# Optimization experiments

Measured on AMD Instinct MI355X. Metric: run time of the kernel, lower is better.

Reference implementation:

```python
import jax, jax.numpy as jnp
import numpy as np

NUM_HEADS = 12
NUM_LANDMARKS = 64
PINV_ITERS = 6


def moore_penrose_iter_pinv(x, iters=PINV_ITERS):
    # x: [..., m, m]
    abs_x = jnp.abs(x)
    col = abs_x.sum(axis=-1)
    row = abs_x.sum(axis=-2)
    z = jnp.swapaxes(x, -1, -2) / (jnp.max(col) * jnp.max(row))
    I = jnp.eye(x.shape[-1], dtype=x.dtype)
    for _ in range(iters):
        xz = x @ z
        z = 0.25 * z @ (13.0 * I - xz @ (15.0 * I - xz @ (7.0 * I - xz)))
    return z


def setup_inputs() -> dict:
    key = jax.random.key(0)
    k1, k2, k3, k4 = jax.random.split(key, 4)
    B, N, C = 2, 2048, 768
    x = jax.random.normal(k1, (B, N, C), dtype=jnp.float32)
    w_qkv = jax.random.normal(k2, (3 * C, C), dtype=jnp.float32) * 0.02
    w_proj = jax.random.normal(k3, (C, C), dtype=jnp.float32) * 0.02
    b_proj = jax.random.normal(k4, (C,), dtype=jnp.float32) * 0.02
    return {"x": x, "w_qkv": w_qkv, "w_proj": w_proj, "b_proj": b_proj}


def reference(x, w_qkv, w_proj, b_proj):
    B, N, C = x.shape
    H = NUM_HEADS
    m = NUM_LANDMARKS
    d = C // H
    scale = d ** -0.5
    original_N = N

    rem = N % m
    if rem > 0:  # pad at the FRONT of the sequence, as in the torch code
        x = jnp.pad(x, ((0, 0), (m - rem, 0), (0, 0)))
        N = x.shape[1]

    qkv = x @ w_qkv.T  # [B, N, 3C]
    q, k, v = jnp.split(qkv, 3, axis=-1)
    # [B, N, C] -> [B, H, N, d]
    to_heads = lambda t: t.reshape(B, N, H, d).transpose(0, 2, 1, 3)
    q, k, v = to_heads(q), to_heads(k), to_heads(v)
    q = q * scale

    l = N // m  # segment length per landmark (N is a multiple of m after padding)
    # '(n l) d -> n d' mean over l: landmarks [B, H, m, d]
    q_landmarks = q.reshape(B, H, m, l, d).mean(axis=3)
    k_landmarks = k.reshape(B, H, m, l, d).mean(axis=3)

    sim1 = jnp.einsum('bhnd,bhmd->bhnm', q, k_landmarks)          # [B,H,N,m]
    sim2 = jnp.einsum('bhid,bhjd->bhij', q_landmarks, k_landmarks)  # [B,H,m,m]
    sim3 = jnp.einsum('bhmd,bhnd->bhmn', q_landmarks, k)          # [B,H,m,N]

    attn1 = jax.nn.softmax(sim1, axis=-1)
    attn2 = jax.nn.softmax(sim2, axis=-1)
    attn3 = jax.nn.softmax(sim3, axis=-1)

    attn2_inv = moore_penrose_iter_pinv(attn2, PINV_ITERS)

    attn = (attn1 @ attn2_inv) @ attn3            # [B,H,N,N] full attention map
    out = attn1 @ (attn2_inv @ (attn3 @ v))       # [B,H,N,d]

    out = out.transpose(0, 2, 1, 3).reshape(B, N, C)
    out = out[:, -original_N:]
    out = out @ w_proj.T + b_proj
    return out, attn
```

## Files before the change

### kernel.cpp

```cpp
#include <hip/hip_runtime.h>
#include <math.h>

#define BQ 2
#define NQ 2048
#define CQ 768
#define HQ 12
#define DQ 64
#define MQ 64
#define LQ 32
#define C3 2304
#define BH 24
#define BN 4096

typedef short bf16x8 __attribute__((ext_vector_type(8)));
typedef float f32x4 __attribute__((ext_vector_type(4)));

__device__ inline void atomicMaxPosF(float* addr, float v) {
  atomicMax((int*)addr, __float_as_int(v));
}

__device__ inline void f2pair(float f, ushort& hi, ushort& lo) {
  union { float f; unsigned u; } a; a.f = f;
  hi = (ushort)(a.u >> 16);
  union { unsigned u; float f; } h; h.u = ((unsigned)hi) << 16;
  union { float f; unsigned u; } b; b.f = f - h.f;
  lo = (ushort)(b.u >> 16);
}

__device__ inline int swzb(int row, int kbyte) {
  return row * 128 + (kbyte ^ ((row & 7) << 4));
}

__device__ inline bf16x8 ldfrag(const ushort* plane, int row, int kbyte) {
  return *(const bf16x8*)((const char*)plane + swzb(row, kbyte));
}

__device__ inline void stage_nt(const float* __restrict__ src, int ld,
                                ushort* ph, ushort* pl, int t) {
#pragma unroll
  for (int rep = 0; rep < 4; ++rep) {
    int idx = t + rep * 256;
    int row = idx >> 4, f4 = idx & 15;
    float4 v = *(const float4*)(src + (size_t)row * ld + f4 * 4);
    ushort h0, h1, h2, h3, l0, l1, l2, l3;
    f2pair(v.x, h0, l0); f2pair(v.y, h1, l1);
    f2pair(v.z, h2, l2); f2pair(v.w, h3, l3);
    int byt = row * 128 + ((f4 * 8) ^ ((row & 7) << 4));
    *(ushort4*)((char*)ph + byt) = make_ushort4(h0, h1, h2, h3);
    *(ushort4*)((char*)pl + byt) = make_ushort4(l0, l1, l2, l3);
  }
}

__device__ inline void stage_nn(const float* __restrict__ src, int ld,
                                ushort* ph, ushort* pl, int t) {
#pragma unroll
  for (int rep = 0; rep < 4; ++rep) {
    int idx = t + rep * 256;
    int krow = idx >> 4, f4 = idx & 15;
    float4 v = *(const float4*)(src + (size_t)krow * ld + f4 * 4);
    float vv[4] = {v.x, v.y, v.z, v.w};
#pragma unroll
    for (int c = 0; c < 4; ++c) {
      int n = f4 * 4 + c;
      ushort hi, lo;
      f2pair(vv[c], hi, lo);
      int byt = n * 128 + ((krow * 2) ^ ((n & 7) << 4));
      *(ushort*)((char*)ph + byt) = hi;
      *(ushort*)((char*)pl + byt) = lo;
    }
  }
}

__device__ inline void tile_mma(const ushort* Ah, const ushort* Al,
                                const ushort* Bh, const ushort* Bl,
                                f32x4 acc[2][2], int lane, int wm, int wn) {
  bf16x8 aH[2][2], aL[2][2], bH[2][2], bL[2][2];
#pragma unroll
  for (int mi = 0; mi < 2; ++mi)
#pragma unroll
    for (int ki = 0; ki < 2; ++ki) {
      int kb = ki * 64 + ((lane >> 4) * 16);
      int ra = wm * 32 + mi * 16 + (lane & 15);
      int rb = wn * 32 + mi * 16 + (lane & 15);
      aH[mi][ki] = ldfrag(Ah, ra, kb);
      aL[mi][ki] = ldfrag(Al, ra, kb);
      bH[mi][ki] = ldfrag(Bh, rb, kb);
      bL[mi][ki] = ldfrag(Bl, rb, kb);
    }
#pragma unroll
  for (int mi = 0; mi < 2; ++mi)
#pragma unroll
    for (int ni = 0; ni < 2; ++ni)
#pragma unroll
      for (int ki = 0; ki < 2; ++ki) {
        acc[mi][ni] = __builtin_amdgcn_mfma_f32_16x16x32_bf16(
            aH[mi][ki], bH[ni][ki], acc[mi][ni], 0, 0, 0);
        acc[mi][ni] = __builtin_amdgcn_mfma_f32_16x16x32_bf16(
            aH[mi][ki], bL[ni][ki], acc[mi][ni], 0, 0, 0);
        acc[mi][ni] = __builtin_amdgcn_mfma_f32_16x16x32_bf16(
            aL[mi][ki], bH[ni][ki], acc[mi][ni], 0, 0, 0);
      }
}

__global__ __launch_bounds__(256) void gemm_nt_mfma(
    const float* __restrict__ X, const float* __restrict__ W,
    const float* __restrict__ bias, float* __restrict__ Y,
    int Kdim, int ldx, int ldw, int ldy, int qscale)
{
  __shared__ __align__(16) ushort lds[16384];
  ushort* Ah = lds; ushort* Al = lds + 4096;
  ushort* Bh = lds + 8192; ushort* Bl = lds + 12288;
  const int t = threadIdx.x;
  const int r0 = blockIdx.x * 64, c0 = blockIdx.y * 64;
  const int lane = t & 63, wv = t >> 6, wm = wv >> 1, wn = wv & 1;
  f32x4 z = {0.f, 0.f, 0.f, 0.f};
  f32x4 acc[2][2] = {{z, z}, {z, z}};
  for (int k0 = 0; k0 < Kdim; k0 += 64) {
    stage_nt(X + (size_t)r0 * ldx + k0, ldx, Ah, Al, t);
    stage_nt(W + (size_t)c0 * ldw + k0, ldw, Bh, Bl, t);
    __syncthreads();
    tile_mma(Ah, Al, Bh, Bl, acc, lane, wm, wn);
    __syncthreads();
  }
#pragma unroll
  for (int mi = 0; mi < 2; ++mi)
#pragma unroll
    for (int ni = 0; ni < 2; ++ni) {
      int row = r0 + wm * 32 + mi * 16 + (lane >> 4) * 4;
      int col = c0 + wn * 32 + ni * 16 + (lane & 15);
      float badd = bias ? bias[col] : 0.0f;
      float sc = (qscale && col < CQ) ? 0.125f : 1.0f;
#pragma unroll
      for (int r = 0; r < 4; ++r)
        Y[(size_t)(row + r) * ldy + col] = acc[mi][ni][r] * sc + badd;
    }
}

__global__ __launch_bounds__(256) void gemm_heads_mfma(
    const float* __restrict__ A, const float* __restrict__ Bsrc,
    float* __restrict__ Cm,
    int kTilesPerSplit, int transB, int nBH,
    long long sAb, long long sAh, int lda,
    long long sBb, long long sBh, int ldb,
    long long sCb, long long sCh, int ldc, long long sCsplit)
{
  __shared__ __align__(16) ushort lds[16384];
  ushort* Ah = lds; ushort* Al = lds + 4096;
  ushort* Bh = lds + 8192; ushort* Bl = lds + 12288;
  const int t = threadIdx.x;
  const int z = blockIdx.z;
  const int split = z / nBH;
  const int bh = z % nBH;
  const int b = bh / HQ, h = bh % HQ;
  const float* Ap = A + (size_t)b * sAb + (size_t)h * sAh;
  const float* Bp = Bsrc + (size_t)b * sBb + (size_t)h * sBh;
  float* Cp = Cm + (size_t)b * sCb + (size_t)h * sCh + (size_t)split * sCsplit;
  const int m0 = blockIdx.x * 64, n0 = blockIdx.y * 64;
  const int lane = t & 63, wv = t >> 6, wm = wv >> 1, wn = wv & 1;
  f32x4 zz = {0.f, 0.f, 0.f, 0.f};
  f32x4 acc[2][2] = {{zz, zz}, {zz, zz}};
  const int kbase = split * kTilesPerSplit * 64;
  for (int kt = 0; kt < kTilesPerSplit; ++kt) {
    int k0 = kbase + kt * 64;
    stage_nt(Ap + (size_t)m0 * lda + k0, lda, Ah, Al, t);
    if (transB)
      stage_nt(Bp + (size_t)n0 * ldb + k0, ldb, Bh, Bl, t);
    else
      stage_nn(Bp + (size_t)k0 * ldb + n0, ldb, Bh, Bl, t);
    __syncthreads();
    tile_mma(Ah, Al, Bh, Bl, acc, lane, wm, wn);
    __syncthreads();
  }
#pragma unroll
  for (int mi = 0; mi < 2; ++mi)
#pragma unroll
    for (int ni = 0; ni < 2; ++ni) {
      int row = m0 + wm * 32 + mi * 16 + (lane >> 4) * 4;
      int col = n0 + wn * 32 + ni * 16 + (lane & 15);
#pragma unroll
      for (int r = 0; r < 4; ++r)
        Cp[(size_t)(row + r) * ldc + col] = acc[mi][ni][r];
    }
}

__global__ void landmarks_kernel(const float* __restrict__ qkv,
                                 float* __restrict__ ql, float* __restrict__ kl)
{
  int idx = blockIdx.x * 256 + threadIdx.x;
  int sel = idx / 98304;
  int r = idx % 98304;
  int bh = r / 4096;
  int b = bh / HQ, h = bh % HQ;
  int i = (r % 4096) / 64;
  int dd = r & 63;
  const float* base = qkv + (size_t)(b * NQ + i * LQ) * C3 + sel * CQ + h * 64 + dd;
  float s = 0.f;
#pragma unroll
  for (int j = 0; j < LQ; ++j) s += base[(size_t)j * C3];
  float* outp = sel ? kl : ql;
  outp[bh * 4096 + i * 64 + dd] = s * (1.0f / 32.0f);
}

__global__ __launch_bounds__(256) void attn2_prep(
    const float* __restrict__ ql, const float* __restrict__ kl,
    float* __restrict__ attn2, float* __restrict__ scal)
{
  __shared__ float Q[64][68], Kl[64][68], S[64][68];
  __shared__ float red[128];
  const int bh = blockIdx.x;
  const int t = threadIdx.x;
#pragma unroll
  for (int rep = 0; rep < 4; ++rep) {
    int idx = t + rep * 256;
    int row = idx >> 4, f4 = idx & 15;
    *(float4*)&Q[row][f4 * 4] = *(const float4*)(ql + (size_t)bh * 4096 + row * 64 + f4 * 4);
    *(float4*)&Kl[row][f4 * 4] = *(const float4*)(kl + (size_t)bh * 4096 + row * 64 + f4 * 4);
  }
  __syncthreads();
  {
    int i = t >> 2;
    int jb = (t & 3) * 16;
    for (int jj = 0; jj < 16; ++jj) {
      int j = jb + jj;
      float s2 = 0.f;
#pragma unroll
      for (int kk = 0; kk < 64; ++kk) s2 = fmaf(Q[i][kk], Kl[j][kk], s2);
      S[i][j] = s2;
    }
  }
  __syncthreads();
  if (t < 64) {
    float mx = -INFINITY;
    for (int j = 0; j < 64; ++j) mx = fmaxf(mx, S[t][j]);
    float sum = 0.f;
    for (int j = 0; j < 64; ++j) { float e = expf(S[t][j] - mx); S[t][j] = e; sum += e; }
    float inv = 1.0f / sum;
    float rs = 0.f;
    for (int j = 0; j < 64; ++j) { float v = S[t][j] * inv; S[t][j] = v; rs += v; }
    red[t] = rs;
  }
  __syncthreads();
  if (t < 64) {
    float cs = 0.f;
    for (int i = 0; i < 64; ++i) cs += S[i][t];
    red[64 + t] = cs;
  }
  __syncthreads();
  if (t == 0) {
    float m1 = red[0], m2 = red[64];
    for (int j = 1; j < 64; ++j) { m1 = fmaxf(m1, red[j]); m2 = fmaxf(m2, red[64 + j]); }
    atomicMaxPosF(scal + 0, m1);
    atomicMaxPosF(scal + 1, m2);
  }
  for (int idx = t; idx < 4096; idx += 256)
    attn2[(size_t)bh * 4096 + idx] = S[idx >> 6][idx & 63];
}

__device__ inline void mm64x(float (*D)[68], const float (*A)[68], const float (*B)[68],
                             int t, float scale)
{
  const int lane = t & 63, wv = t >> 6;
  float bcol[64];
#pragma unroll
  for (int kk = 0; kk < 64; ++kk) bcol[kk] = B[kk][lane];
#pragma unroll
  for (int rr = 0; rr < 4; ++rr) {
    int i = wv * 4 + rr;
    float acc2 = 0.f;
#pragma unroll
    for (int kk = 0; kk < 64; ++kk) acc2 = fmaf(A[i][kk], bcol[kk], acc2);
    D[i][lane] = acc2 * scale;
  }
}

__global__ __launch_bounds__(1024) void pinv_kernel(
    const float* __restrict__ attn2, const float* __restrict__ scal,
    float* __restrict__ zinv)
{
  __shared__ float X[64][68], Z[64][68], P[64][68], Q[64][68], R[64][68];
  const int bh = blockIdx.x;
  const int t = threadIdx.x;
  const float denom = scal[0] * scal[1];
#pragma unroll
  for (int rep = 0; rep < 4; ++rep) {
    int idx = t + rep * 1024;
    X[idx >> 6][idx & 63] = attn2[(size_t)bh * 4096 + idx];
  }
  __syncthreads();
#pragma unroll
  for (int rep = 0; rep < 4; ++rep) {
    int idx = t + rep * 1024;
    int i = idx >> 6, j = idx & 63;
    Z[j][i] = X[i][j] / denom;
  }
  for (int it = 0; it < 6; ++it) {
    __syncthreads();
    mm64x(P, X, Z, t, 1.0f);
    __syncthreads();
    for (int idx = t; idx < 4096; idx += 1024) {
      int i = idx >> 6, j = idx & 63;
      Q[i][j] = (i == j ? 7.0f : 0.0f) - P[i][j];
    }
    __syncthreads();
    mm64x(R, P, Q, t, 1.0f);
    __syncthreads();
    for (int idx = t; idx < 4096; idx += 1024) {
      int i = idx >> 6, j = idx & 63;
      Q[i][j] = (i == j ? 15.0f : 0.0f) - R[i][j];
    }
    __syncthreads();
    mm64x(R, P, Q, t, 1.0f);
    __syncthreads();
    for (int idx = t; idx < 4096; idx += 1024) {
      int i = idx >> 6, j = idx & 63;
      Q[i][j] = (i == j ? 13.0f : 0.0f) - R[i][j];
    }
    __syncthreads();
    mm64x(P, Z, Q, t, 0.25f);
    __syncthreads();
    for (int idx = t; idx < 4096; idx += 1024) {
      int i = idx >> 6, j = idx & 63;
      Z[i][j] = P[i][j];
    }
  }
  __syncthreads();
  for (int idx = t; idx < 4096; idx += 1024)
    zinv[(size_t)bh * 4096 + idx] = Z[idx >> 6][idx & 63];
}

__global__ __launch_bounds__(256) void attn1_kernel(
    const float* __restrict__ qkv, const float* __restrict__ kl,
    float* __restrict__ attn1)
{
  __shared__ float qs[64][68], klt[64][68];
  const int n0 = blockIdx.x * 64;
  const int bh = blockIdx.y;
  const int b = bh / HQ, h = bh % HQ;
  const int t = threadIdx.x;
#pragma unroll
  for (int rep = 0; rep < 4; ++rep) {
    int idx = t + rep * 256;
    int row = idx >> 4, f4 = idx & 15;
    *(float4*)&qs[row][f4 * 4] =
        *(const float4*)(qkv + (size_t)(b * NQ + n0 + row) * C3 + h * 64 + f4 * 4);
    float4 kv = *(const float4*)(kl + (size_t)bh * 4096 + row * 64 + f4 * 4);
    klt[f4 * 4 + 0][row] = kv.x; klt[f4 * 4 + 1][row] = kv.y;
    klt[f4 * 4 + 2][row] = kv.z; klt[f4 * 4 + 3][row] = kv.w;
  }
  __syncthreads();
  const int lane = t & 63, wv = t >> 6;
  float bcol[64];
#pragma unroll
  for (int kk = 0; kk < 64; ++kk) bcol[kk] = klt[kk][lane];
  for (int rr = 0; rr < 16; ++rr) {
    int i = wv * 16 + rr;
    float s = 0.f;
#pragma unroll
    for (int kk = 0; kk < 64; ++kk) s = fmaf(qs[i][kk], bcol[kk], s);
    float mx = s;
#pragma unroll
    for (int off = 32; off; off >>= 1) mx = fmaxf(mx, __shfl_xor(mx, off));
    float e = expf(s - mx);
    float sum = e;
#pragma unroll
    for (int off = 32; off; off >>= 1) sum += __shfl_xor(sum, off);
    attn1[(size_t)bh * 131072 + (size_t)(n0 + i) * 64 + lane] = e / sum;
  }
}

__global__ __launch_bounds__(256) void softmax2048(float* __restrict__ buf)
{
  __shared__ float red[8];
  const size_t base = (size_t)blockIdx.x * 2048;
  const int t = threadIdx.x;
  const int wv = t >> 6, lane = t & 63;
  float v[8];
  float mx = -INFINITY;
#pragma unroll
  for (int r = 0; r < 8; ++r) {
    v[r] = buf[base + t + r * 256];
    mx = fmaxf(mx, v[r]);
  }
#pragma unroll
  for (int off = 32; off; off >>= 1) mx = fmaxf(mx, __shfl_xor(mx, off));
  if (lane == 0) red[wv] = mx;
  __syncthreads();
  mx = fmaxf(fmaxf(red[0], red[1]), fmaxf(red[2], red[3]));
  float sum = 0.f;
#pragma unroll
  for (int r = 0; r < 8; ++r) { v[r] = expf(v[r] - mx); sum += v[r]; }
#pragma unroll
  for (int off = 32; off; off >>= 1) sum += __shfl_xor(sum, off);
  if (lane == 0) red[4 + wv] = sum;
  __syncthreads();
  float total = (red[4] + red[5]) + (red[6] + red[7]);
  float inv = 1.0f / total;
#pragma unroll
  for (int r = 0; r < 8; ++r) buf[base + t + r * 256] = v[r] * inv;
}

__global__ void reduce8_kernel(const float* __restrict__ part, float* __restrict__ outp)
{
  int idx = blockIdx.x * 256 + threadIdx.x;
  float s = 0.f;
#pragma unroll
  for (int r = 0; r < 8; ++r) s += part[(size_t)r * 98304 + idx];
  outp[idx] = s;
}

__global__ void init_scal(float* s)
{
  if (threadIdx.x < 2) s[threadIdx.x] = 0.0f;
}

extern "C" void kernel_launch(void* const* d_in, const int* in_sizes, int n_in,
                              void* d_out, int out_size, void* d_ws, size_t ws_size,
                              hipStream_t stream)
{
  const float* x = (const float*)d_in[0];
  const float* w_qkv = (const float*)d_in[1];
  const float* w_proj = (const float*)d_in[2];
  const float* b_proj = (const float*)d_in[3];
  float* out = (float*)d_out;
  float* attnO = out + (size_t)BQ * NQ * CQ;

  float* ws = (float*)d_ws;
  float* QL = ws;
  float* KL = QL + 98304;
  float* A2 = KL + 98304;
  float* ZI = A2 + 98304;
  float* AT1 = ZI + 98304;
  float* TB = AT1 + 3145728;
  float* W3V = TB + 3145728;
  float* UU = W3V + 98304;
  float* SC = UU + 98304;

  float* QKV = attnO;
  float* AT3 = QKV + 9437184;
  float* OH = AT3 + 3145728;
  float* W3P = OH + 3145728;

  init_scal<<<1, 64, 0, stream>>>(SC);

  gemm_nt_mfma<<<dim3(64, 36), 256, 0, stream>>>(x, w_qkv, nullptr, QKV,
                                                 CQ, CQ, CQ, C3, 1);
  landmarks_kernel<<<768, 256, 0, stream>>>(QKV, QL, KL);
  attn2_prep<<<24, 256, 0, stream>>>(QL, KL, A2, SC);
  pinv_kernel<<<24, 1024, 0, stream>>>(A2, SC, ZI);
  attn1_kernel<<<dim3(32, 24), 256, 0, stream>>>(QKV, KL, AT1);
  gemm_heads_mfma<<<dim3(1, 32, 24), 256, 0, stream>>>(
      QL, QKV + CQ, AT3, 1, 1, 24,
      (long long)HQ * 4096, 4096, 64,
      (long long)NQ * C3, 64, C3,
      (long long)HQ * 131072, 131072, 2048, 0);
  softmax2048<<<1536, 256, 0, stream>>>(AT3);
  gemm_heads_mfma<<<dim3(1, 1, 192), 256, 0, stream>>>(
      AT3, QKV + 2 * CQ, W3P, 4, 0, 24,
      (long long)HQ * 131072, 131072, 2048,
      (long long)NQ * C3, 64, C3,
      (long long)HQ * 4096, 4096, 64, (long long)24 * 4096);
  reduce8_kernel<<<384, 256, 0, stream>>>(W3P, W3V);
  gemm_heads_mfma<<<dim3(1, 1, 24), 256, 0, stream>>>(
      ZI, W3V, UU, 1, 0, 24,
      (long long)HQ * 4096, 4096, 64,
      (long long)HQ * 4096, 4096, 64,
      (long long)HQ * 4096, 4096, 64, 0);
  gemm_heads_mfma<<<dim3(32, 1, 24), 256, 0, stream>>>(
      AT1, UU, OH, 1, 0, 24,
      (long long)HQ * 131072, 131072, 64,
      (long long)HQ * 4096, 4096, 64,
      (long long)NQ * CQ, 64, CQ, 0);
  gemm_nt_mfma<<<dim3(64, 12), 256, 0, stream>>>(OH, w_proj, b_proj, out,
                                                 CQ, CQ, CQ, CQ, 0);
  gemm_heads_mfma<<<dim3(1, 32, 24), 256, 0, stream>>>(
      ZI, AT3, TB, 1, 0, 24,
      (long long)HQ * 4096, 4096, 64,
      (long long)HQ * 131072, 131072, 2048,
      (long long)HQ * 131072, 131072, 2048, 0);
  gemm_heads_mfma<<<dim3(32, 32, 24), 256, 0, stream>>>(
      AT1, TB, attnO, 1, 0, 24,
      (long long)HQ * 131072, 131072, 64,
      (long long)HQ * 131072, 131072, 2048,
      (long long)HQ * 4194304LL, 4194304, 2048, 0);
}
```

Measured before the change: 440.8 us.

## Pre-split operands into bf16 hi/lo planes and use 128x128 async-LDS GEMM

Adds a gemm_bt3 kernel that reads operands already split into bf16 hi/lo planes and loads them with global_load_lds into 128x128 tiles. The QKV projection, the output projection and the big N×N attention-map GEMM now use it. attn1 and the transposed (attn2_inv@attn3) matrix are emitted directly as hi/lo planes. The output projection is re-associated by folding w_proj into attn2_inv@attn3@v per head (w_proj·U), so the out-projection becomes a single K=768 GEMM from attn1. The aim is to cut the repeated fp32-to-bf16 splitting, raise data reuse per tile, and drop the OH intermediate, at the cost of extra conversion and transpose kernels and more scratch memory.

```diff
diff --git a/kernel.cpp b/kernel.cpp
--- a/kernel.cpp
+++ b/kernel.cpp
@@ -27,6 +27,107 @@
   lo = (ushort)(b.u >> 16);
 }
 
+__device__ inline void stage_plane(const ushort* __restrict__ g, int ld,
+                                   ushort* l, int t) {
+#pragma unroll
+  for (int i = 0; i < 4; ++i) {
+    int flat = t + i * 256;
+    int row = flat >> 3;
+    int ch = (flat & 7) ^ (row & 7);
+    __builtin_amdgcn_global_load_lds(
+        (const __attribute__((address_space(1))) void*)(g + (size_t)row * ld + ch * 8),
+        (__attribute__((address_space(3))) void*)(l + flat * 8), 16, 0, 0);
+  }
+}
+
+__device__ inline bf16x8 rdfrag(const ushort* p, int row, int kb) {
+  return *(const bf16x8*)((const char*)p + row * 128 + (kb ^ ((row & 7) << 4)));
+}
+
+__global__ __launch_bounds__(256) void gemm_bt3(
+    const ushort* __restrict__ Ah, const ushort* __restrict__ Al,
+    const ushort* __restrict__ Bh, const ushort* __restrict__ Bl,
+    const float* __restrict__ bias, float* __restrict__ C,
+    int Kdim, int lda, int ldb, int ldc, int qscale, int zH,
+    long long sAb, long long sAh, long long sBb, long long sBh,
+    long long sCb, long long sCh)
+{
+  __shared__ __align__(16) ushort lds[32768];
+  ushort* LAh = lds;
+  ushort* LAl = lds + 8192;
+  ushort* LBh = lds + 16384;
+  ushort* LBl = lds + 24576;
+  const int t = threadIdx.x;
+  const int z = blockIdx.z;
+  const int b = z / zH, h = z % zH;
+  const size_t aoff = (size_t)b * sAb + (size_t)h * sAh + (size_t)blockIdx.x * 128 * lda;
+  const size_t boff = (size_t)b * sBb + (size_t)h * sBh + (size_t)blockIdx.y * 128 * ldb;
+  const ushort* pAh = Ah + aoff;
+  const ushort* pAl = Al + aoff;
+  const ushort* pBh = Bh + boff;
+  const ushort* pBl = Bl + boff;
+  float* Cp = C + (size_t)b * sCb + (size_t)h * sCh;
+  const int lane = t & 63, wv = t >> 6, wm = wv >> 1, wn = wv & 1;
+  f32x4 zz = {0.f, 0.f, 0.f, 0.f};
+  f32x4 acc[4][4] = {{zz, zz, zz, zz}, {zz, zz, zz, zz},
+                     {zz, zz, zz, zz}, {zz, zz, zz, zz}};
+  for (int k0 = 0; k0 < Kdim; k0 += 64) {
+    stage_plane(pAh + k0, lda, LAh, t);
+    stage_plane(pAl + k0, lda, LAl, t);
+    stage_plane(pBh + k0, ldb, LBh, t);
+    stage_plane(pBl + k0, ldb, LBl, t);
+    __syncthreads();
+#pragma unroll
+    for (int kh = 0; kh < 2; ++kh) {
+      const int kb = kh * 64 + ((lane >> 4) * 16);
+      bf16x8 aH[4], aL[4], bHf[4], bLf[4];
+#pragma unroll
+      for (int i = 0; i < 4; ++i) {
+        int ra = wm * 64 + i * 16 + (lane & 15);
+        int rb = wn * 64 + i * 16 + (lane & 15);
+        aH[i] = rdfrag(LAh, ra, kb);
+        aL[i] = rdfrag(LAl, ra, kb);
+        bHf[i] = rdfrag(LBh, rb, kb);
+        bLf[i] = rdfrag(LBl, rb, kb);
+      }
+#pragma unroll
+      for (int i = 0; i < 4; ++i)
+#pragma unroll
+        for (int j = 0; j < 4; ++j) {
+          acc[i][j] = __builtin_amdgcn_mfma_f32_16x16x32_bf16(aH[i], bHf[j], acc[i][j], 0, 0, 0);
+          acc[i][j] = __builtin_amdgcn_mfma_f32_16x16x32_bf16(aH[i], bLf[j], acc[i][j], 0, 0, 0);
+          acc[i][j] = __builtin_amdgcn_mfma_f32_16x16x32_bf16(aL[i], bHf[j], acc[i][j], 0, 0, 0);
+        }
+    }
+    __syncthreads();
+  }
+#pragma unroll
+  for (int i = 0; i < 4; ++i)
+#pragma unroll
+    for (int j = 0; j < 4; ++j) {
+      int row = blockIdx.x * 128 + wm * 64 + i * 16 + (lane >> 4) * 4;
+      int col = blockIdx.y * 128 + wn * 64 + j * 16 + (lane & 15);
+      float badd = bias ? bias[col] : 0.0f;
+      float sc = (qscale && col < CQ) ? 0.125f : 1.0f;
+#pragma unroll
+      for (int r = 0; r < 4; ++r)
+        Cp[(size_t)(row + r) * ldc + col] = acc[i][j][r] * sc + badd;
+    }
+}
+
+__global__ void convert_planes(const float* __restrict__ src, ushort* __restrict__ hi,
+                               ushort* __restrict__ lo, int n4)
+{
+  int i = blockIdx.x * 256 + threadIdx.x;
+  if (i >= n4) return;
+  float4 v = ((const float4*)src)[i];
+  ushort4 H, L;
+  f2pair(v.x, H.x, L.x); f2pair(v.y, H.y, L.y);
+  f2pair(v.z, H.z, L.z); f2pair(v.w, H.w, L.w);
+  ((ushort4*)hi)[i] = H;
+  ((ushort4*)lo)[i] = L;
+}
+
 __device__ inline int swzb(int row, int kbyte) {
   return row * 128 + (kbyte ^ ((row & 7) << 4));
 }
@@ -102,47 +203,14 @@
       }
 }
 
-__global__ __launch_bounds__(256) void gemm_nt_mfma(
-    const float* __restrict__ X, const float* __restrict__ W,
-    const float* __restrict__ bias, float* __restrict__ Y,
-    int Kdim, int ldx, int ldw, int ldy, int qscale)
-{
-  __shared__ __align__(16) ushort lds[16384];
-  ushort* Ah = lds; ushort* Al = lds + 4096;
-  ushort* Bh = lds + 8192; ushort* Bl = lds + 12288;
-  const int t = threadIdx.x;
-  const int r0 = blockIdx.x * 64, c0 = blockIdx.y * 64;
-  const int lane = t & 63, wv = t >> 6, wm = wv >> 1, wn = wv & 1;
-  f32x4 z = {0.f, 0.f, 0.f, 0.f};
-  f32x4 acc[2][2] = {{z, z}, {z, z}};
-  for (int k0 = 0; k0 < Kdim; k0 += 64) {
-    stage_nt(X + (size_t)r0 * ldx + k0, ldx, Ah, Al, t);
-    stage_nt(W + (size_t)c0 * ldw + k0, ldw, Bh, Bl, t);
-    __syncthreads();
-    tile_mma(Ah, Al, Bh, Bl, acc, lane, wm, wn);
-    __syncthreads();
-  }
-#pragma unroll
-  for (int mi = 0; mi < 2; ++mi)
-#pragma unroll
-    for (int ni = 0; ni < 2; ++ni) {
-      int row = r0 + wm * 32 + mi * 16 + (lane >> 4) * 4;
-      int col = c0 + wn * 32 + ni * 16 + (lane & 15);
-      float badd = bias ? bias[col] : 0.0f;
-      float sc = (qscale && col < CQ) ? 0.125f : 1.0f;
-#pragma unroll
-      for (int r = 0; r < 4; ++r)
-        Y[(size_t)(row + r) * ldy + col] = acc[mi][ni][r] * sc + badd;
-    }
-}
-
 __global__ __launch_bounds__(256) void gemm_heads_mfma(
     const float* __restrict__ A, const float* __restrict__ Bsrc,
     float* __restrict__ Cm,
     int kTilesPerSplit, int transB, int nBH,
     long long sAb, long long sAh, int lda,
     long long sBb, long long sBh, int ldb,
-    long long sCb, long long sCh, int ldc, long long sCsplit)
+    long long sCb, long long sCh, int ldc, long long sCsplit,
+    ushort* __restrict__ Hout, ushort* __restrict__ Lout)
 {
   __shared__ __align__(16) ushort lds[16384];
   ushort* Ah = lds; ushort* Al = lds + 4096;
@@ -154,7 +222,6 @@
   const int b = bh / HQ, h = bh % HQ;
   const float* Ap = A + (size_t)b * sAb + (size_t)h * sAh;
   const float* Bp = Bsrc + (size_t)b * sBb + (size_t)h * sBh;
-  float* Cp = Cm + (size_t)b * sCb + (size_t)h * sCh + (size_t)split * sCsplit;
   const int m0 = blockIdx.x * 64, n0 = blockIdx.y * 64;
   const int lane = t & 63, wv = t >> 6, wm = wv >> 1, wn = wv & 1;
   f32x4 zz = {0.f, 0.f, 0.f, 0.f};
@@ -171,16 +238,36 @@
     tile_mma(Ah, Al, Bh, Bl, acc, lane, wm, wn);
     __syncthreads();
   }
-#pragma unroll
-  for (int mi = 0; mi < 2; ++mi)
-#pragma unroll
-    for (int ni = 0; ni < 2; ++ni) {
-      int row = m0 + wm * 32 + mi * 16 + (lane >> 4) * 4;
-      int col = n0 + wn * 32 + ni * 16 + (lane & 15);
-#pragma unroll
-      for (int r = 0; r < 4; ++r)
-        Cp[(size_t)(row + r) * ldc + col] = acc[mi][ni][r];
-    }
+  if (Hout) {
+    ushort* Hp = Hout + (size_t)b * sCb + (size_t)h * sCh + (size_t)split * sCsplit;
+    ushort* Lp = Lout + (size_t)b * sCb + (size_t)h * sCh + (size_t)split * sCsplit;
+#pragma unroll
+    for (int mi = 0; mi < 2; ++mi)
+#pragma unroll
+      for (int ni = 0; ni < 2; ++ni) {
+        int row = m0 + wm * 32 + mi * 16 + (lane >> 4) * 4;
+        int col = n0 + wn * 32 + ni * 16 + (lane & 15);
+#pragma unroll
+        for (int r = 0; r < 4; ++r) {
+          ushort hi, lo;
+          f2pair(acc[mi][ni][r], hi, lo);
+          Hp[(size_t)(row + r) * ldc + col] = hi;
+          Lp[(size_t)(row + r) * ldc + col] = lo;
+        }
+      }
+  } else {
+    float* Cp = Cm + (size_t)b * sCb + (size_t)h * sCh + (size_t)split * sCsplit;
+#pragma unroll
+    for (int mi = 0; mi < 2; ++mi)
+#pragma unroll
+      for (int ni = 0; ni < 2; ++ni) {
+        int row = m0 + wm * 32 + mi * 16 + (lane >> 4) * 4;
+        int col = n0 + wn * 32 + ni * 16 + (lane & 15);
+#pragma unroll
+        for (int r = 0; r < 4; ++r)
+          Cp[(size_t)(row + r) * ldc + col] = acc[mi][ni][r];
+      }
+  }
 }
 
 __global__ void landmarks_kernel(const float* __restrict__ qkv,
@@ -330,7 +417,7 @@
 
 __global__ __launch_bounds__(256) void attn1_kernel(
     const float* __restrict__ qkv, const float* __restrict__ kl,
-    float* __restrict__ attn1)
+    ushort* __restrict__ A1h, ushort* __restrict__ A1l)
 {
   __shared__ float qs[64][68], klt[64][68];
   const int n0 = blockIdx.x * 64;
@@ -364,7 +451,12 @@
     float sum = e;
 #pragma unroll
     for (int off = 32; off; off >>= 1) sum += __shfl_xor(sum, off);
-    attn1[(size_t)bh * 131072 + (size_t)(n0 + i) * 64 + lane] = e / sum;
+    float v = e / sum;
+    ushort hi, lo;
+    f2pair(v, hi, lo);
+    size_t o = ((size_t)(b * NQ + n0 + i)) * CQ + h * 64 + lane;
+    A1h[o] = hi;
+    A1l[o] = lo;
   }
 }
 
@@ -408,6 +500,34 @@
   outp[idx] = s;
 }
 
+__global__ __launch_bounds__(256) void transpose_T(
+    const float* __restrict__ TBm, ushort* __restrict__ TTh, ushort* __restrict__ TTl)
+{
+  __shared__ float S[64][65];
+  const int bh = blockIdx.y;
+  const int n0 = blockIdx.x * 64;
+  const int t = threadIdx.x;
+  const float* src = TBm + (size_t)bh * 131072 + n0;
+#pragma unroll
+  for (int i = 0; i < 16; ++i) {
+    int idx = t + i * 256;
+    int m = idx >> 6, nn = idx & 63;
+    S[m][nn] = src[(size_t)m * 2048 + nn];
+  }
+  __syncthreads();
+  ushort* dh = TTh + (size_t)bh * 131072 + (size_t)n0 * 64;
+  ushort* dl = TTl + (size_t)bh * 131072 + (size_t)n0 * 64;
+#pragma unroll
+  for (int i = 0; i < 16; ++i) {
+    int idx = t + i * 256;
+    int nn = idx >> 6, m = idx & 63;
+    ushort hi, lo;
+    f2pair(S[m][nn], hi, lo);
+    dh[(size_t)nn * 64 + m] = hi;
+    dl[(size_t)nn * 64 + m] = lo;
+  }
+}
+
 __global__ void init_scal(float* s)
 {
   if (threadIdx.x < 2) s[threadIdx.x] = 0.0f;
@@ -422,64 +542,88 @@
   const float* w_proj = (const float*)d_in[2];
   const float* b_proj = (const float*)d_in[3];
   float* out = (float*)d_out;
-  float* attnO = out + (size_t)BQ * NQ * CQ;
+  float* R = out + (size_t)BQ * NQ * CQ;
+
+  float* QKV = R;
+  float* AT3 = R + 9437184;
+  float* TBm = R + 12582912;
+  float* W3P = R + 15728640;
+  float* W3V = R + 16515072;
+  float* UU  = R + 16613376;
+  ushort* xp_h = (ushort*)(R + 16711680);
+  ushort* xp_l = xp_h + 3145728;
+  ushort* wq_h = xp_l + 3145728;
+  ushort* wq_l = wq_h + 1769472;
+  ushort* gt_h = wq_l + 1769472;
+  ushort* gt_l = gt_h + 1179648;
 
   float* ws = (float*)d_ws;
   float* QL = ws;
   float* KL = QL + 98304;
   float* A2 = KL + 98304;
   float* ZI = A2 + 98304;
-  float* AT1 = ZI + 98304;
-  float* TB = AT1 + 3145728;
-  float* W3V = TB + 3145728;
-  float* UU = W3V + 98304;
-  float* SC = UU + 98304;
-
-  float* QKV = attnO;
-  float* AT3 = QKV + 9437184;
-  float* OH = AT3 + 3145728;
-  float* W3P = OH + 3145728;
+  float* SC = ZI + 98304;
+  ushort* a1_h = (ushort*)(SC + 32);
+  ushort* a1_l = a1_h + 3145728;
+  ushort* tt_h = a1_l + 3145728;
+  ushort* tt_l = tt_h + 3145728;
 
   init_scal<<<1, 64, 0, stream>>>(SC);
 
-  gemm_nt_mfma<<<dim3(64, 36), 256, 0, stream>>>(x, w_qkv, nullptr, QKV,
-                                                 CQ, CQ, CQ, C3, 1);
+  convert_planes<<<3072, 256, 0, stream>>>(x, xp_h, xp_l, 786432);
+  convert_planes<<<1728, 256, 0, stream>>>(w_qkv, wq_h, wq_l, 442368);
+
+  gemm_bt3<<<dim3(32, 18, 1), 256, 0, stream>>>(
+      xp_h, xp_l, wq_h, wq_l, nullptr, QKV,
+      CQ, CQ, CQ, C3, 1, 1, 0, 0, 0, 0, 0, 0);
+
   landmarks_kernel<<<768, 256, 0, stream>>>(QKV, QL, KL);
   attn2_prep<<<24, 256, 0, stream>>>(QL, KL, A2, SC);
   pinv_kernel<<<24, 1024, 0, stream>>>(A2, SC, ZI);
-  attn1_kernel<<<dim3(32, 24), 256, 0, stream>>>(QKV, KL, AT1);
+  attn1_kernel<<<dim3(32, 24), 256, 0, stream>>>(QKV, KL, a1_h, a1_l);
+
   gemm_heads_mfma<<<dim3(1, 32, 24), 256, 0, stream>>>(
       QL, QKV + CQ, AT3, 1, 1, 24,
       (long long)HQ * 4096, 4096, 64,
       (long long)NQ * C3, 64, C3,
-      (long long)HQ * 131072, 131072, 2048, 0);
+      (long long)HQ * 131072, 131072, 2048, 0, nullptr, nullptr);
   softmax2048<<<1536, 256, 0, stream>>>(AT3);
+
   gemm_heads_mfma<<<dim3(1, 1, 192), 256, 0, stream>>>(
       AT3, QKV + 2 * CQ, W3P, 4, 0, 24,
       (long long)HQ * 131072, 131072, 2048,
       (long long)NQ * C3, 64, C3,
-      (long long)HQ * 4096, 4096, 64, (long long)24 * 4096);
+      (long long)HQ * 4096, 4096, 64, (long long)24 * 4096, nullptr, nullptr);
   reduce8_kernel<<<384, 256, 0, stream>>>(W3P, W3V);
+
   gemm_heads_mfma<<<dim3(1, 1, 24), 256, 0, stream>>>(
       ZI, W3V, UU, 1, 0, 24,
       (long long)HQ * 4096, 4096, 64,
       (long long)HQ * 4096, 4096, 64,
-      (long long)HQ * 4096, 4096, 64, 0);
-  gemm_heads_mfma<<<dim3(32, 1, 24), 256, 0, stream>>>(
-      AT1, UU, OH, 1, 0, 24,
-      (long long)HQ * 131072, 131072, 64,
+      (long long)HQ * 4096, 4096, 64, 0, nullptr, nullptr);
+
+  gemm_heads_mfma<<<dim3(12, 1, 24), 256, 0, stream>>>(
+      w_proj, UU, nullptr, 1, 1, 24,
+      0, 64, CQ,
       (long long)HQ * 4096, 4096, 64,
-      (long long)NQ * CQ, 64, CQ, 0);
-  gemm_nt_mfma<<<dim3(64, 12), 256, 0, stream>>>(OH, w_proj, b_proj, out,
-                                                 CQ, CQ, CQ, CQ, 0);
+      (long long)CQ * CQ, 64, CQ, 0, gt_h, gt_l);
+
   gemm_heads_mfma<<<dim3(1, 32, 24), 256, 0, stream>>>(
-      ZI, AT3, TB, 1, 0, 24,
+      ZI, AT3, TBm, 1, 0, 24,
       (long long)HQ * 4096, 4096, 64,
       (long long)HQ * 131072, 131072, 2048,
-      (long long)HQ * 131072, 131072, 2048, 0);
-  gemm_heads_mfma<<<dim3(32, 32, 24), 256, 0, stream>>>(
-      AT1, TB, attnO, 1, 0, 24,
-      (long long)HQ * 131072, 131072, 64,
-      (long long)HQ * 131072, 131072, 2048,
-      (long long)HQ * 4194304LL, 4194304, 2048, 0);
-}
+      (long long)HQ * 131072, 131072, 2048, 0, nullptr, nullptr);
+  transpose_T<<<dim3(32, 24), 256, 0, stream>>>(TBm, tt_h, tt_l);
+
+  gemm_bt3<<<dim3(16, 6, 2), 256, 0, stream>>>(
+      a1_h, a1_l, gt_h, gt_l, b_proj, out,
+      CQ, CQ, CQ, CQ, 0, 1,
+      (long long)NQ * CQ, 0, (long long)CQ * CQ, 0, (long long)NQ * CQ, 0);
+
+  gemm_bt3<<<dim3(16, 16, 24), 256, 0, stream>>>(
+      a1_h, a1_l, tt_h, tt_l, nullptr, R,
+      64, CQ, 64, 2048, 0, HQ,
+      (long long)NQ * CQ, 64,
+      (long long)HQ * 131072, 131072,
+      (long long)HQ * 4194304LL, 4194304);
+}
```

Result: faster. 381.5 us, median of 3 (-13.5%).
